# Performance work log

Hardware: AMD Instinct MI355X
Metric: run time of the kernel (lower is better)

## Reference

```python
import jax, jax.numpy as jnp
import numpy as np

N_NODES = 100000
N_EDGES = 1600000
NUM_GRAPHS = 1024
D_IN = 128
D_HID = 128
D_OUT = 2
LN_EPS = 1e-5


def setup_inputs() -> dict:
    key = jax.random.key(0)
    ks = jax.random.split(key, 10)
    x = jax.random.normal(ks[0], (N_NODES, D_IN), dtype=jnp.float32)
    edge_index = jax.random.randint(ks[1], (2, N_EDGES), 0, N_NODES, dtype=jnp.int64)
    batch = jnp.sort(jax.random.randint(ks[2], (N_NODES,), 0, NUM_GRAPHS, dtype=jnp.int64))
    s = 0.05  # weight scale to keep activations sane
    return {
        "x": x,
        "edge_index": edge_index,
        "batch": batch,
        "W1l": jax.random.normal(ks[3], (D_HID, D_IN), dtype=jnp.float32) * s,
        "b1l": jnp.zeros((D_HID,), dtype=jnp.float32),
        "W1r": jax.random.normal(ks[4], (D_HID, D_IN), dtype=jnp.float32) * s,
        "W2l": jax.random.normal(ks[5], (D_HID, D_HID), dtype=jnp.float32) * s,
        "b2l": jnp.zeros((D_HID,), dtype=jnp.float32),
        "W2r": jax.random.normal(ks[6], (D_HID, D_HID), dtype=jnp.float32) * s,
        "ln_g": jnp.ones((D_HID,), dtype=jnp.float32),
        "ln_b": jnp.zeros((D_HID,), dtype=jnp.float32),
        "Wlin": jax.random.normal(ks[7], (D_OUT, D_HID), dtype=jnp.float32) * s,
        "blin": jnp.zeros((D_OUT,), dtype=jnp.float32),
    }


def _sage_conv(x, src, dst, Wl, bl, Wr):
    # PyG SAGEConv with mean aggregation: lin_l(mean_{j in N(i)} x_j) + lin_r(x_i)
    msg_sum = jax.ops.segment_sum(x[src], dst, num_segments=N_NODES)
    deg = jax.ops.segment_sum(jnp.ones((src.shape[0], 1), x.dtype), dst, num_segments=N_NODES)
    agg = msg_sum / jnp.maximum(deg, 1.0)  # isolated nodes -> 0
    return agg @ Wl.T + bl + x @ Wr.T  # lin_r has no bias (PyG default)


def reference(x, edge_index, batch, W1l, b1l, W1r, W2l, b2l, W2r, ln_g, ln_b, Wlin, blin):
    src, dst = edge_index[0], edge_index[1]
    h = jax.nn.relu(_sage_conv(x, src, dst, W1l, b1l, W1r))
    h = jax.nn.relu(_sage_conv(h, src, dst, W2l, b2l, W2r))
    # global_add_pool over graphs
    g = jax.ops.segment_sum(h, batch, num_segments=NUM_GRAPHS)  # [G, D_HID]
    # LayerNorm over last dim
    mu = jnp.mean(g, axis=-1, keepdims=True)
    var = jnp.var(g, axis=-1, keepdims=True)
    gn = (g - mu) * jax.lax.rsqrt(var + LN_EPS) * ln_g + ln_b
    return gn @ Wlin.T + blin  # [G, D_OUT]
```

## Files before the change

### kernel.cpp

```cpp
#include <hip/hip_runtime.h>
#include <hip/hip_bf16.h>
#include <hip/hip_fp8.h>

#define N_NODES   100000
#define N_EDGES   1600000
#define NUM_GRAPHS 1024
#define D         128
#define LN_EPS    1e-5f
#define NBUCKETS  391
#define CAP       4864
#define CHUNK     4096

typedef __attribute__((ext_vector_type(8))) short short8;
typedef __attribute__((ext_vector_type(4))) float floatx4;
typedef __attribute__((ext_vector_type(2))) float f32x2;

static __device__ __forceinline__ float bf2f(unsigned int u) {
    return __uint_as_float(u << 16);
}
static __device__ __forceinline__ unsigned short f2bf(float f) {
    __hip_bfloat16 h = __float2bfloat16(f);
    return *reinterpret_cast<unsigned short*>(&h);
}
static __device__ __forceinline__ void acc4(f32x2* acc, uint4 v) {
    acc[0] += (f32x2){__uint_as_float(v.x << 16), __uint_as_float(v.x & 0xffff0000u)};
    acc[1] += (f32x2){__uint_as_float(v.y << 16), __uint_as_float(v.y & 0xffff0000u)};
    acc[2] += (f32x2){__uint_as_float(v.z << 16), __uint_as_float(v.z & 0xffff0000u)};
    acc[3] += (f32x2){__uint_as_float(v.w << 16), __uint_as_float(v.w & 0xffff0000u)};
}

#if __has_builtin(__builtin_amdgcn_cvt_pk_f32_fp8)
#define UNPK_FP8(x, w) __builtin_amdgcn_cvt_pk_f32_fp8((x), (w))
#else
static __device__ __forceinline__ f32x2 unpk_fp8_sw(unsigned x, bool w) {
    unsigned s = w ? (x >> 16) : (x & 0xffffu);
    __hip_fp8_e4m3 a, b;
    *reinterpret_cast<unsigned char*>(&a) = (unsigned char)(s & 0xff);
    *reinterpret_cast<unsigned char*>(&b) = (unsigned char)((s >> 8) & 0xff);
    return (f32x2){(float)a, (float)b};
}
#define UNPK_FP8(x, w) unpk_fp8_sw((x), (w))
#endif

#if __has_builtin(__builtin_amdgcn_cvt_pk_fp8_f32)
#define PK_FP8(a, b, old, w) ((unsigned)__builtin_amdgcn_cvt_pk_fp8_f32((a), (b), (int)(old), (w)))
#else
static __device__ __forceinline__ unsigned pk_fp8_sw(float a, float b) {
    __hip_fp8_e4m3 fa = (__hip_fp8_e4m3)a;
    __hip_fp8_e4m3 fb = (__hip_fp8_e4m3)b;
    return (unsigned)*reinterpret_cast<unsigned char*>(&fa) |
           ((unsigned)*reinterpret_cast<unsigned char*>(&fb) << 8);
}
#define PK_FP8(a, b, old, w) ((w) ? ((((unsigned)(old)) & 0xffffu) | (pk_fp8_sw((a),(b)) << 16)) \
                                  : ((((unsigned)(old)) & 0xffff0000u) | pk_fp8_sw((a),(b))))
#endif

#define GLOAD16(g, l) __builtin_amdgcn_global_load_lds( \
    (const __attribute__((address_space(1))) void*)(g), \
    (__attribute__((address_space(3))) void*)(l), 16, 0, 0)

__global__ __launch_bounds__(256)
void prep_kernel(const float* __restrict__ x, unsigned short* __restrict__ xbf,
                 unsigned* __restrict__ xf8,
                 const float* __restrict__ W1l, const float* __restrict__ W1r,
                 const float* __restrict__ W2l, const float* __restrict__ W2r,
                 unsigned short* __restrict__ Wc1, unsigned short* __restrict__ Wc2,
                 int* __restrict__ cursor) {
    int i = blockIdx.x * 256 + threadIdx.x;
    float4 v = reinterpret_cast<const float4*>(x)[i];
    ushort4 o;
    o.x = f2bf(v.x); o.y = f2bf(v.y); o.z = f2bf(v.z); o.w = f2bf(v.w);
    reinterpret_cast<ushort4*>(xbf)[i] = o;
    unsigned p = PK_FP8(v.x, v.y, 0u, false);
    p = PK_FP8(v.z, v.w, p, true);
    xf8[i] = p;
    if (blockIdx.x < 256) {
        int layer = i >> 15;
        int rem = i & 32767;
        int c = rem >> 8;
        int k = rem & 255;
        const float* Wl = layer ? W2l : W1l;
        const float* Wr = layer ? W2r : W1r;
        unsigned short* dst = layer ? Wc2 : Wc1;
        float wv = (k < 128) ? Wl[c * 128 + k] : Wr[c * 128 + (k - 128)];
        dst[c * 256 + k] = f2bf(wv);
    }
    if (blockIdx.x == 256) {
        for (int b = threadIdx.x; b < NBUCKETS; b += 256)
            cursor[b] = b * CAP;
        if (threadIdx.x < 32)
            xf8[(size_t)N_NODES * 32 + threadIdx.x] = 0u;
    }
}

__global__ __launch_bounds__(256)
void cvt_h1_kernel(const unsigned short* __restrict__ h1, uint2* __restrict__ h1f8) {
    int i = blockIdx.x * 256 + threadIdx.x;
    uint4 v = reinterpret_cast<const uint4*>(h1)[i];
    float c0 = __uint_as_float(v.x << 16), c1 = __uint_as_float(v.x & 0xffff0000u);
    float c2 = __uint_as_float(v.y << 16), c3 = __uint_as_float(v.y & 0xffff0000u);
    float c4 = __uint_as_float(v.z << 16), c5 = __uint_as_float(v.z & 0xffff0000u);
    float c6 = __uint_as_float(v.w << 16), c7 = __uint_as_float(v.w & 0xffff0000u);
    unsigned lo = PK_FP8(c0, c1, 0u, false);
    lo = PK_FP8(c2, c3, lo, true);
    unsigned hi = PK_FP8(c4, c5, 0u, false);
    hi = PK_FP8(c6, c7, hi, true);
    h1f8[i] = make_uint2(lo, hi);
}

__global__ __launch_bounds__(256)
void bin_scatter_kernel(const int* __restrict__ src, const int* __restrict__ dst,
                        int* __restrict__ cursor, unsigned* __restrict__ binned) {
    __shared__ int cnt[NBUCKETS];
    __shared__ int base[NBUCKETS];
    int chunkBase = blockIdx.x * CHUNK;
    for (int i = threadIdx.x; i < NBUCKETS; i += 256) cnt[i] = 0;
    __syncthreads();
    int es[16], ed[16], lofs[16];
    #pragma unroll
    for (int j = 0; j < 16; ++j) {
        int e = chunkBase + j * 256 + threadIdx.x;
        if (e < N_EDGES) {
            es[j] = src[e];
            ed[j] = dst[e];
            lofs[j] = atomicAdd(&cnt[ed[j] >> 8], 1);
        }
    }
    __syncthreads();
    for (int i = threadIdx.x; i < NBUCKETS; i += 256) {
        int c = cnt[i];
        base[i] = c ? atomicAdd(&cursor[i], c) : 0;
    }
    __syncthreads();
    #pragma unroll
    for (int j = 0; j < 16; ++j) {
        int e = chunkBase + j * 256 + threadIdx.x;
        if (e < N_EDGES) {
            int b = ed[j] >> 8;
            int pos = base[b] + lofs[j];
            if (pos < (b + 1) * CAP)
                binned[pos] = ((unsigned)(ed[j] & 255) << 17) | (unsigned)es[j];
        }
    }
}

__global__ __launch_bounds__(256)
void bucket_build_kernel(const unsigned* __restrict__ binned, const int* __restrict__ cursor,
                         int2* __restrict__ row_info, int* __restrict__ src_sorted) {
    __shared__ int scnt[256];
    __shared__ int sscan[256];
    int b = blockIdx.x;
    int t = threadIdx.x;
    int lo = b * CAP;
    int hi = cursor[b];
    int cap_end = lo + CAP;
    if (hi > cap_end) hi = cap_end;
    scnt[t] = 0;
    __syncthreads();
    unsigned rec[19];
    short rnk[19];
    #pragma unroll
    for (int i = 0; i < 19; ++i) {
        int e = lo + t + i * 256;
        if (e < hi) {
            unsigned r = binned[e];
            rec[i] = r;
            rnk[i] = (short)atomicAdd(&scnt[r >> 17], 1);
        }
    }
    __syncthreads();
    int v = scnt[t];
    sscan[t] = v;
    __syncthreads();
    for (int off = 1; off < 256; off <<= 1) {
        int a = (t >= off) ? sscan[t - off] : 0;
        __syncthreads();
        sscan[t] += a;
        __syncthreads();
    }
    int ex = sscan[t] - v;
    int node = b * 256 + t;
    if (node < N_NODES) row_info[node] = make_int2(lo + ex, v);
    scnt[t] = ex;
    __syncthreads();
    #pragma unroll
    for (int i = 0; i < 19; ++i) {
        int e = lo + t + i * 256;
        if (e < hi) {
            unsigned r = rec[i];
            src_sorted[lo + scnt[r >> 17] + rnk[i]] = (int)(r & 0x1FFFFu);
        }
    }
}

__global__ __launch_bounds__(256)
void aggregate_kernel(const unsigned char* __restrict__ feat8,
                      const int* __restrict__ src_sorted,
                      const int2* __restrict__ row_info,
                      unsigned short* __restrict__ aggout) {
    int bid = blockIdx.x;
    int xcd = bid & 7;
    int idx = bid >> 3;
    int lb  = (xcd < 2) ? xcd * 782 + idx : 1564 + (xcd - 2) * 781 + idx;
    int tid  = threadIdx.x;
    int wave = tid >> 6;
    int lane = tid & 63;
    int l16  = lane & 15;
    int grpbase = lane & 48;
    int node = lb * 16 + wave * 4 + (lane >> 4);
    int2 ri = row_info[node];
    int s = ri.x, deg = ri.y;
    int dmax = deg;
    dmax = max(dmax, __shfl_xor(dmax, 16, 64));
    dmax = max(dmax, __shfl_xor(dmax, 32, 64));
    unsigned chb = (unsigned)l16 * 8;
    f32x2 a0[4], a1[4];
    #pragma unroll
    for (int i = 0; i < 4; ++i) { a0[i] = (f32x2){0.f, 0.f}; a1[i] = (f32x2){0.f, 0.f}; }

    for (int c0 = 0; c0 < dmax; c0 += 16) {
        int si = src_sorted[s + c0 + l16];
        int rel = deg - c0;
        int rend = dmax - c0; if (rend > 16) rend = 16;
        int r = 0;
        for (; r + 2 <= rend; r += 2) {
            int u0 = __shfl(si, grpbase + r, 64);
            int u1 = __shfl(si, grpbase + r + 1, 64);
            u0 = (r < rel) ? u0 : N_NODES;
            u1 = (r + 1 < rel) ? u1 : N_NODES;
            uint2 v0 = *(const uint2*)(feat8 + (((unsigned)u0 << 7) + chb));
            uint2 v1 = *(const uint2*)(feat8 + (((unsigned)u1 << 7) + chb));
            a0[0] += UNPK_FP8(v0.x, false);
            a0[1] += UNPK_FP8(v0.x, true);
            a0[2] += UNPK_FP8(v0.y, false);
            a0[3] += UNPK_FP8(v0.y, true);
            a1[0] += UNPK_FP8(v1.x, false);
            a1[1] += UNPK_FP8(v1.x, true);
            a1[2] += UNPK_FP8(v1.y, false);
            a1[3] += UNPK_FP8(v1.y, true);
        }
        if (r < rend) {
            int u0 = __shfl(si, grpbase + r, 64);
            u0 = (r < rel) ? u0 : N_NODES;
            uint2 v0 = *(const uint2*)(feat8 + (((unsigned)u0 << 7) + chb));
            a0[0] += UNPK_FP8(v0.x, false);
            a0[1] += UNPK_FP8(v0.x, true);
            a0[2] += UNPK_FP8(v0.y, false);
            a0[3] += UNPK_FP8(v0.y, true);
        }
    }
    float inv = 1.f / (float)(deg > 1 ? deg : 1);
    f32x2 t0 = (a0[0] + a1[0]) * inv;
    f32x2 t1 = (a0[1] + a1[1]) * inv;
    f32x2 t2 = (a0[2] + a1[2]) * inv;
    f32x2 t3 = (a0[3] + a1[3]) * inv;
    uint4 o;
    o.x = (unsigned)f2bf(t0.x) | ((unsigned)f2bf(t0.y) << 16);
    o.y = (unsigned)f2bf(t1.x) | ((unsigned)f2bf(t1.y) << 16);
    o.z = (unsigned)f2bf(t2.x) | ((unsigned)f2bf(t2.y) << 16);
    o.w = (unsigned)f2bf(t3.x) | ((unsigned)f2bf(t3.y) << 16);
    *(uint4*)(aggout + (size_t)node * 128 + l16 * 8) = o;
}

__global__ __launch_bounds__(256)
void gemm_kernel(const unsigned short* __restrict__ A1,
                 const unsigned short* __restrict__ A2,
                 const unsigned short* __restrict__ Wcat,
                 const float* __restrict__ bias,
                 unsigned short* __restrict__ out) {
    __shared__ unsigned char sm[2][12288];
    int tid  = threadIdx.x;
    int w    = tid >> 6;
    int lane = tid & 63;
    int quad = lane >> 4, m = lane & 15;
    int nodeBase = blockIdx.x * 64;
    int gm = (m & 3) ^ ((m >> 2) & 3);
    int qo = ((quad ^ gm) & 3) * 16;

    int arow = w * 16 + (lane >> 2);
    int ga   = (arow & 3) ^ ((arow >> 2) & 3);
    int ua   = (lane & 3) ^ ga;
    int ra   = nodeBase + arow; if (ra > N_NODES - 1) ra = N_NODES - 1;
    int col0 = w * 32 + (lane >> 2);
    int col1 = col0 + 16;
    int u0 = (lane & 3) ^ ((col0 & 3) ^ ((col0 >> 2) & 3));
    int u1 = (lane & 3) ^ ((col1 & 3) ^ ((col1 >> 2) & 3));
    const char* a1c = (const char*)A1;
    const char* a2c = (const char*)A2;
    const char* wcc = (const char*)Wcat;

    floatx4 acc[4][2];
    #pragma unroll
    for (int a = 0; a < 4; ++a)
        #pragma unroll
        for (int b = 0; b < 2; ++b) acc[a][b] = (floatx4){0.f, 0.f, 0.f, 0.f};

#define STAGE(kc, buf) do {                                                      \
        const char* asrc = ((kc) < 4) ? a1c : a2c;                               \
        int kb = ((kc) & 3) * 64;                                               \
        GLOAD16(asrc + (size_t)ra * 256 + kb + ua * 16, &sm[buf][w * 1024]);     \
        int kw = (kc) * 64;                                                     \
        GLOAD16(wcc + (size_t)col0 * 512 + kw + u0 * 16, &sm[buf][4096 + (w*2)*1024]);     \
        GLOAD16(wcc + (size_t)col1 * 512 + kw + u1 * 16, &sm[buf][4096 + (w*2+1)*1024]);   \
    } while (0)

    STAGE(0, 0);
    __syncthreads();
    #pragma unroll
    for (int kc = 0; kc < 8; ++kc) {
        int buf = kc & 1;
        if (kc < 7) STAGE(kc + 1, buf ^ 1);
        const char* As = (const char*)&sm[buf][0];
        const char* Ws = (const char*)&sm[buf][4096];
        short8 afr[4], bfr[2];
        #pragma unroll
        for (int nb = 0; nb < 4; ++nb)
            afr[nb] = *(const short8*)(As + (nb * 16 + m) * 64 + qo);
        #pragma unroll
        for (int cb = 0; cb < 2; ++cb)
            bfr[cb] = *(const short8*)(Ws + (w * 32 + cb * 16 + m) * 64 + qo);
        #pragma unroll
        for (int nb = 0; nb < 4; ++nb)
            #pragma unroll
            for (int cb = 0; cb < 2; ++cb)
                acc[nb][cb] = __builtin_amdgcn_mfma_f32_16x16x32_bf16(afr[nb], bfr[cb], acc[nb][cb], 0, 0, 0);
        if (kc < 7) __syncthreads();
    }
#undef STAGE

    #pragma unroll
    for (int cb = 0; cb < 2; ++cb) {
        int col = w * 32 + cb * 16 + m;
        float bv = bias[col];
        #pragma unroll
        for (int nb = 0; nb < 4; ++nb) {
            #pragma unroll
            for (int rr = 0; rr < 4; ++rr) {
                int row = nodeBase + nb * 16 + quad * 4 + rr;
                if (row < N_NODES) {
                    float v = acc[nb][cb][rr] + bv;
                    v = v > 0.f ? v : 0.f;
                    out[(size_t)row * 128 + col] = f2bf(v);
                }
            }
        }
    }
}

__global__ __launch_bounds__(256)
void pool_ln_out_kernel(const unsigned short* __restrict__ h2,
                        const int* __restrict__ batch,
                        const float* __restrict__ ln_g, const float* __restrict__ ln_b,
                        const float* __restrict__ Wlin, const float* __restrict__ blin,
                        float* __restrict__ out) {
    int g = blockIdx.x;
    int t = threadIdx.x;
    int lane = t & 63, w = t >> 6;
    __shared__ int se[2];
    if (t < 2) {
        int target = g + t;
        int lo = 0, hi = N_NODES;
        while (lo < hi) {
            int mid = (lo + hi) >> 1;
            if (batch[mid] < target) lo = mid + 1; else hi = mid;
        }
        se[t] = lo;
    }
    __syncthreads();
    int s = se[0], e = se[1];
    int ns = t >> 4;
    int chg = t & 15;
    f32x2 a[4];
    a[0] = a[1] = a[2] = a[3] = (f32x2){0.f, 0.f};
    for (int n = s + ns; n < e; n += 16) {
        uint4 v = *(const uint4*)(h2 + (size_t)n * 128 + chg * 8);
        acc4(a, v);
    }
    #pragma unroll
    for (int i = 0; i < 4; ++i) {
        a[i].x += __shfl_xor(a[i].x, 16, 64);
        a[i].y += __shfl_xor(a[i].y, 16, 64);
        a[i].x += __shfl_xor(a[i].x, 32, 64);
        a[i].y += __shfl_xor(a[i].y, 32, 64);
    }
    __shared__ float sw[4][128];
    if (lane < 16) {
        #pragma unroll
        for (int k = 0; k < 4; ++k) {
            sw[w][chg * 8 + 2 * k]     = a[k].x;
            sw[w][chg * 8 + 2 * k + 1] = a[k].y;
        }
    }
    __syncthreads();
    __shared__ float red[128];
    float sum = 0.f;
    if (t < 128) {
        sum = sw[0][t] + sw[1][t] + sw[2][t] + sw[3][t];
        red[t] = sum;
    }
    __syncthreads();
    for (int off = 64; off > 0; off >>= 1) {
        if (t < off) red[t] += red[t + off];
        __syncthreads();
    }
    float mu = red[0] * (1.f / 128.f);
    __syncthreads();
    float dv = sum - mu;
    if (t < 128) red[t] = dv * dv;
    __syncthreads();
    for (int off = 64; off > 0; off >>= 1) {
        if (t < off) red[t] += red[t + off];
        __syncthreads();
    }
    float var = red[0] * (1.f / 128.f);
    __syncthreads();
    __shared__ float r0[128], r1[128];
    if (t < 128) {
        float gn = dv * rsqrtf(var + LN_EPS) * ln_g[t] + ln_b[t];
        r0[t] = gn * Wlin[t];
        r1[t] = gn * Wlin[128 + t];
    }
    __syncthreads();
    for (int off = 64; off > 0; off >>= 1) {
        if (t < off) { r0[t] += r0[t + off]; r1[t] += r1[t + off]; }
        __syncthreads();
    }
    if (t == 0) {
        out[g * 2 + 0] = r0[0] + blin[0];
        out[g * 2 + 1] = r1[0] + blin[1];
    }
}

extern "C" void kernel_launch(void* const* d_in, const int* in_sizes, int n_in,
                              void* d_out, int out_size, void* d_ws, size_t ws_size,
                              hipStream_t stream) {
    const float* x    = (const float*)d_in[0];
    const int*   ei   = (const int*)d_in[1];
    const int*   batch= (const int*)d_in[2];
    const float* W1l  = (const float*)d_in[3];
    const float* b1l  = (const float*)d_in[4];
    const float* W1r  = (const float*)d_in[5];
    const float* W2l  = (const float*)d_in[6];
    const float* b2l  = (const float*)d_in[7];
    const float* W2r  = (const float*)d_in[8];
    const float* ln_g = (const float*)d_in[9];
    const float* ln_b = (const float*)d_in[10];
    const float* Wlin = (const float*)d_in[11];
    const float* blin = (const float*)d_in[12];
    float* out = (float*)d_out;

    char* ws = (char*)d_ws;
    size_t off = 0;
    auto alloc = [&](size_t bytes) {
        char* p = ws + off;
        off = (off + bytes + 255) & ~(size_t)255;
        return p;
    };
    unsigned short* xbf  = (unsigned short*)alloc((size_t)N_NODES * D * 2);
    unsigned short* aggb = (unsigned short*)alloc((size_t)N_NODES * D * 2);
    unsigned short* h1   = (unsigned short*)alloc((size_t)N_NODES * D * 2);
    unsigned*       xf8  = (unsigned*)alloc((size_t)N_NODES * D + 128);
    unsigned short* Wc1  = (unsigned short*)alloc(128 * 256 * 2);
    unsigned short* Wc2  = (unsigned short*)alloc(128 * 256 * 2);
    int2* row_info   = (int2*)alloc((size_t)N_NODES * 8);
    int* src_sorted  = (int*)alloc(((size_t)NBUCKETS * CAP + 8192) * 4);
    int* cursor      = (int*)alloc(NBUCKETS * 4);
    unsigned* binned = (unsigned*)aggb;
    uint2* h1f8      = (uint2*)xf8;

    const int* srcI = ei;
    const int* dstI = ei + N_EDGES;

    prep_kernel<<<12500, 256, 0, stream>>>(x, xbf, xf8, W1l, W1r, W2l, W2r, Wc1, Wc2, cursor);
    bin_scatter_kernel<<<(N_EDGES + CHUNK - 1) / CHUNK, 256, 0, stream>>>(srcI, dstI, cursor, binned);
    bucket_build_kernel<<<NBUCKETS, 256, 0, stream>>>(binned, cursor, row_info, src_sorted);

    aggregate_kernel<<<6250, 256, 0, stream>>>((const unsigned char*)xf8, src_sorted, row_info, aggb);
    gemm_kernel<<<1563, 256, 0, stream>>>(aggb, xbf, Wc1, b1l, h1);
    cvt_h1_kernel<<<6250, 256, 0, stream>>>(h1, h1f8);
    aggregate_kernel<<<6250, 256, 0, stream>>>((const unsigned char*)h1f8, src_sorted, row_info, aggb);
    gemm_kernel<<<1563, 256, 0, stream>>>(aggb, h1, Wc2, b2l, xbf);
    pool_ln_out_kernel<<<NUM_GRAPHS, 256, 0, stream>>>(xbf, batch, ln_g, ln_b, Wlin, blin, out);
}
```

Before: 291.2 us.

## Fuse neighbor aggregation into the SAGE GEMM kernel and drop the h1 FP8 conversion

Each of the two layers now runs as one kernel: a block gathers and averages neighbor features for its 64 nodes into shared memory, then runs the MFMA GEMM against the concatenated weights. This removes the round trip of the aggregated bf16 matrix through global memory and one kernel launch per layer. The separate h1-to-FP8 conversion is also dropped, so layer 2 gathers bf16 h1 directly. That doubles the gather bytes for layer 2, and with 32KB of LDS plus the weight buffers per block, fewer blocks may be resident on each CU to hide gather latency.

Result: slower. 359.2 us (+23.3%).

```diff
diff --git a/kernel.cpp b/kernel.cpp
--- a/kernel.cpp
+++ b/kernel.cpp
@@ -15,9 +15,6 @@
 typedef __attribute__((ext_vector_type(4))) float floatx4;
 typedef __attribute__((ext_vector_type(2))) float f32x2;
 
-static __device__ __forceinline__ float bf2f(unsigned int u) {
-    return __uint_as_float(u << 16);
-}
 static __device__ __forceinline__ unsigned short f2bf(float f) {
     __hip_bfloat16 h = __float2bfloat16(f);
     return *reinterpret_cast<unsigned short*>(&h);
@@ -65,7 +62,7 @@
                  const float* __restrict__ W1l, const float* __restrict__ W1r,
                  const float* __restrict__ W2l, const float* __restrict__ W2r,
                  unsigned short* __restrict__ Wc1, unsigned short* __restrict__ Wc2,
-                 int* __restrict__ cursor) {
+                 int* __restrict__ cursor, unsigned short* __restrict__ h1) {
     int i = blockIdx.x * 256 + threadIdx.x;
     float4 v = reinterpret_cast<const float4*>(x)[i];
     ushort4 o;
@@ -90,22 +87,9 @@
             cursor[b] = b * CAP;
         if (threadIdx.x < 32)
             xf8[(size_t)N_NODES * 32 + threadIdx.x] = 0u;
-    }
-}
-
-__global__ __launch_bounds__(256)
-void cvt_h1_kernel(const unsigned short* __restrict__ h1, uint2* __restrict__ h1f8) {
-    int i = blockIdx.x * 256 + threadIdx.x;
-    uint4 v = reinterpret_cast<const uint4*>(h1)[i];
-    float c0 = __uint_as_float(v.x << 16), c1 = __uint_as_float(v.x & 0xffff0000u);
-    float c2 = __uint_as_float(v.y << 16), c3 = __uint_as_float(v.y & 0xffff0000u);
-    float c4 = __uint_as_float(v.z << 16), c5 = __uint_as_float(v.z & 0xffff0000u);
-    float c6 = __uint_as_float(v.w << 16), c7 = __uint_as_float(v.w & 0xffff0000u);
-    unsigned lo = PK_FP8(c0, c1, 0u, false);
-    lo = PK_FP8(c2, c3, lo, true);
-    unsigned hi = PK_FP8(c4, c5, 0u, false);
-    hi = PK_FP8(c6, c7, hi, true);
-    h1f8[i] = make_uint2(lo, hi);
+        if (threadIdx.x < 64)
+            reinterpret_cast<unsigned*>(h1)[(size_t)N_NODES * 64 + threadIdx.x] = 0u;
+    }
 }
 
 __global__ __launch_bounds__(256)
@@ -193,101 +177,126 @@
     }
 }
 
+template <bool FP8>
 __global__ __launch_bounds__(256)
-void aggregate_kernel(const unsigned char* __restrict__ feat8,
-                      const int* __restrict__ src_sorted,
-                      const int2* __restrict__ row_info,
-                      unsigned short* __restrict__ aggout) {
-    int bid = blockIdx.x;
-    int xcd = bid & 7;
-    int idx = bid >> 3;
-    int lb  = (xcd < 2) ? xcd * 782 + idx : 1564 + (xcd - 2) * 781 + idx;
-    int tid  = threadIdx.x;
-    int wave = tid >> 6;
-    int lane = tid & 63;
-    int l16  = lane & 15;
-    int grpbase = lane & 48;
-    int node = lb * 16 + wave * 4 + (lane >> 4);
-    int2 ri = row_info[node];
-    int s = ri.x, deg = ri.y;
-    int dmax = deg;
-    dmax = max(dmax, __shfl_xor(dmax, 16, 64));
-    dmax = max(dmax, __shfl_xor(dmax, 32, 64));
-    unsigned chb = (unsigned)l16 * 8;
-    f32x2 a0[4], a1[4];
-    #pragma unroll
-    for (int i = 0; i < 4; ++i) { a0[i] = (f32x2){0.f, 0.f}; a1[i] = (f32x2){0.f, 0.f}; }
-
-    for (int c0 = 0; c0 < dmax; c0 += 16) {
-        int si = src_sorted[s + c0 + l16];
-        int rel = deg - c0;
-        int rend = dmax - c0; if (rend > 16) rend = 16;
-        int r = 0;
-        for (; r + 2 <= rend; r += 2) {
-            int u0 = __shfl(si, grpbase + r, 64);
-            int u1 = __shfl(si, grpbase + r + 1, 64);
-            u0 = (r < rel) ? u0 : N_NODES;
-            u1 = (r + 1 < rel) ? u1 : N_NODES;
-            uint2 v0 = *(const uint2*)(feat8 + (((unsigned)u0 << 7) + chb));
-            uint2 v1 = *(const uint2*)(feat8 + (((unsigned)u1 << 7) + chb));
-            a0[0] += UNPK_FP8(v0.x, false);
-            a0[1] += UNPK_FP8(v0.x, true);
-            a0[2] += UNPK_FP8(v0.y, false);
-            a0[3] += UNPK_FP8(v0.y, true);
-            a1[0] += UNPK_FP8(v1.x, false);
-            a1[1] += UNPK_FP8(v1.x, true);
-            a1[2] += UNPK_FP8(v1.y, false);
-            a1[3] += UNPK_FP8(v1.y, true);
-        }
-        if (r < rend) {
-            int u0 = __shfl(si, grpbase + r, 64);
-            u0 = (r < rel) ? u0 : N_NODES;
-            uint2 v0 = *(const uint2*)(feat8 + (((unsigned)u0 << 7) + chb));
-            a0[0] += UNPK_FP8(v0.x, false);
-            a0[1] += UNPK_FP8(v0.x, true);
-            a0[2] += UNPK_FP8(v0.y, false);
-            a0[3] += UNPK_FP8(v0.y, true);
-        }
-    }
-    float inv = 1.f / (float)(deg > 1 ? deg : 1);
-    f32x2 t0 = (a0[0] + a1[0]) * inv;
-    f32x2 t1 = (a0[1] + a1[1]) * inv;
-    f32x2 t2 = (a0[2] + a1[2]) * inv;
-    f32x2 t3 = (a0[3] + a1[3]) * inv;
-    uint4 o;
-    o.x = (unsigned)f2bf(t0.x) | ((unsigned)f2bf(t0.y) << 16);
-    o.y = (unsigned)f2bf(t1.x) | ((unsigned)f2bf(t1.y) << 16);
-    o.z = (unsigned)f2bf(t2.x) | ((unsigned)f2bf(t2.y) << 16);
-    o.w = (unsigned)f2bf(t3.x) | ((unsigned)f2bf(t3.y) << 16);
-    *(uint4*)(aggout + (size_t)node * 128 + l16 * 8) = o;
-}
-
-__global__ __launch_bounds__(256)
-void gemm_kernel(const unsigned short* __restrict__ A1,
-                 const unsigned short* __restrict__ A2,
-                 const unsigned short* __restrict__ Wcat,
-                 const float* __restrict__ bias,
-                 unsigned short* __restrict__ out) {
-    __shared__ unsigned char sm[2][12288];
+void fused_layer_kernel(const unsigned char* __restrict__ gat,
+                        const unsigned short* __restrict__ selfA,
+                        const unsigned short* __restrict__ Wcat,
+                        const float* __restrict__ bias,
+                        const int* __restrict__ src_sorted,
+                        const int2* __restrict__ row_info,
+                        unsigned short* __restrict__ out) {
+    __shared__ unsigned char A1s[16384];
+    __shared__ unsigned char A2s[16384];
+    __shared__ unsigned char Wsm[2][8192];
     int tid  = threadIdx.x;
     int w    = tid >> 6;
     int lane = tid & 63;
     int quad = lane >> 4, m = lane & 15;
-    int nodeBase = blockIdx.x * 64;
+    int sub  = quad;
+    int l16  = m;
+    int grpbase = lane & 48;
+    int bid = blockIdx.x;
+    int xcd = bid & 7, idx = bid >> 3;
+    int lb = (xcd < 3) ? xcd * 196 + idx : 588 + (xcd - 3) * 195 + idx;
+    int nodeBase = lb * 64;
+
+    const char* wcc = (const char*)Wcat;
     int gm = (m & 3) ^ ((m >> 2) & 3);
     int qo = ((quad ^ gm) & 3) * 16;
-
-    int arow = w * 16 + (lane >> 2);
-    int ga   = (arow & 3) ^ ((arow >> 2) & 3);
-    int ua   = (lane & 3) ^ ga;
-    int ra   = nodeBase + arow; if (ra > N_NODES - 1) ra = N_NODES - 1;
     int col0 = w * 32 + (lane >> 2);
     int col1 = col0 + 16;
     int u0 = (lane & 3) ^ ((col0 & 3) ^ ((col0 >> 2) & 3));
     int u1 = (lane & 3) ^ ((col1 & 3) ^ ((col1 >> 2) & 3));
-    const char* a1c = (const char*)A1;
-    const char* a2c = (const char*)A2;
-    const char* wcc = (const char*)Wcat;
+
+#define STAGE_W(kc, buf) do {                                                    \
+        int kw = (kc) * 64;                                                      \
+        GLOAD16(wcc + (size_t)col0 * 512 + kw + u0 * 16, &Wsm[buf][(w*2)*1024]);     \
+        GLOAD16(wcc + (size_t)col1 * 512 + kw + u1 * 16, &Wsm[buf][(w*2+1)*1024]);   \
+    } while (0)
+
+    {
+        const char* sc = (const char*)selfA;
+        #pragma unroll
+        for (int j = 0; j < 4; ++j) {
+            int row = w * 16 + j * 4 + (lane >> 4);
+            int node = nodeBase + row; if (node > N_NODES - 1) node = N_NODES - 1;
+            int u = (lane & 15) ^ (row & 15);
+            GLOAD16(sc + (size_t)node * 256 + u * 16, &A2s[w * 4096 + j * 1024]);
+        }
+        STAGE_W(0, 0);
+    }
+
+    for (int round = 0; round < 4; ++round) {
+        int arow = w * 16 + round * 4 + sub;
+        int node = nodeBase + arow;
+        int nn = node < N_NODES ? node : N_NODES - 1;
+        int2 ri = row_info[nn];
+        int s = ri.x;
+        int deg = node < N_NODES ? ri.y : 0;
+        int dmax = deg;
+        dmax = max(dmax, __shfl_xor(dmax, 16, 64));
+        dmax = max(dmax, __shfl_xor(dmax, 32, 64));
+        f32x2 a0[4], a1[4];
+        #pragma unroll
+        for (int i = 0; i < 4; ++i) { a0[i] = (f32x2){0.f, 0.f}; a1[i] = (f32x2){0.f, 0.f}; }
+
+        for (int c0 = 0; c0 < dmax; c0 += 16) {
+            int si = src_sorted[s + c0 + l16];
+            int rel = deg - c0;
+            int rend = dmax - c0; if (rend > 16) rend = 16;
+            int r = 0;
+            for (; r + 2 <= rend; r += 2) {
+                int e0 = __shfl(si, grpbase + r, 64);
+                int e1 = __shfl(si, grpbase + r + 1, 64);
+                e0 = (r < rel) ? e0 : N_NODES;
+                e1 = (r + 1 < rel) ? e1 : N_NODES;
+                if constexpr (FP8) {
+                    uint2 v0 = *(const uint2*)(gat + (((size_t)e0 << 7) + l16 * 8));
+                    uint2 v1 = *(const uint2*)(gat + (((size_t)e1 << 7) + l16 * 8));
+                    a0[0] += UNPK_FP8(v0.x, false);
+                    a0[1] += UNPK_FP8(v0.x, true);
+                    a0[2] += UNPK_FP8(v0.y, false);
+                    a0[3] += UNPK_FP8(v0.y, true);
+                    a1[0] += UNPK_FP8(v1.x, false);
+                    a1[1] += UNPK_FP8(v1.x, true);
+                    a1[2] += UNPK_FP8(v1.y, false);
+                    a1[3] += UNPK_FP8(v1.y, true);
+                } else {
+                    uint4 v0 = *(const uint4*)(gat + (((size_t)e0 << 8) + l16 * 16));
+                    uint4 v1 = *(const uint4*)(gat + (((size_t)e1 << 8) + l16 * 16));
+                    acc4(a0, v0);
+                    acc4(a1, v1);
+                }
+            }
+            if (r < rend) {
+                int e0 = __shfl(si, grpbase + r, 64);
+                e0 = (r < rel) ? e0 : N_NODES;
+                if constexpr (FP8) {
+                    uint2 v0 = *(const uint2*)(gat + (((size_t)e0 << 7) + l16 * 8));
+                    a0[0] += UNPK_FP8(v0.x, false);
+                    a0[1] += UNPK_FP8(v0.x, true);
+                    a0[2] += UNPK_FP8(v0.y, false);
+                    a0[3] += UNPK_FP8(v0.y, true);
+                } else {
+                    uint4 v0 = *(const uint4*)(gat + (((size_t)e0 << 8) + l16 * 16));
+                    acc4(a0, v0);
+                }
+            }
+        }
+        float inv = 1.f / (float)(deg > 1 ? deg : 1);
+        f32x2 t0 = (a0[0] + a1[0]) * inv;
+        f32x2 t1 = (a0[1] + a1[1]) * inv;
+        f32x2 t2 = (a0[2] + a1[2]) * inv;
+        f32x2 t3 = (a0[3] + a1[3]) * inv;
+        uint4 o;
+        o.x = (unsigned)f2bf(t0.x) | ((unsigned)f2bf(t0.y) << 16);
+        o.y = (unsigned)f2bf(t1.x) | ((unsigned)f2bf(t1.y) << 16);
+        o.z = (unsigned)f2bf(t2.x) | ((unsigned)f2bf(t2.y) << 16);
+        o.w = (unsigned)f2bf(t3.x) | ((unsigned)f2bf(t3.y) << 16);
+        *(uint4*)(&A1s[arow * 256 + ((l16 ^ (arow & 15)) << 4)]) = o;
+    }
+    __syncthreads();
 
     floatx4 acc[4][2];
     #pragma unroll
@@ -295,30 +304,19 @@
         #pragma unroll
         for (int b = 0; b < 2; ++b) acc[a][b] = (floatx4){0.f, 0.f, 0.f, 0.f};
 
-#define STAGE(kc, buf) do {                                                      \
-        const char* asrc = ((kc) < 4) ? a1c : a2c;                               \
-        int kb = ((kc) & 3) * 64;                                               \
-        GLOAD16(asrc + (size_t)ra * 256 + kb + ua * 16, &sm[buf][w * 1024]);     \
-        int kw = (kc) * 64;                                                     \
-        GLOAD16(wcc + (size_t)col0 * 512 + kw + u0 * 16, &sm[buf][4096 + (w*2)*1024]);     \
-        GLOAD16(wcc + (size_t)col1 * 512 + kw + u1 * 16, &sm[buf][4096 + (w*2+1)*1024]);   \
-    } while (0)
-
-    STAGE(0, 0);
-    __syncthreads();
     #pragma unroll
     for (int kc = 0; kc < 8; ++kc) {
         int buf = kc & 1;
-        if (kc < 7) STAGE(kc + 1, buf ^ 1);
-        const char* As = (const char*)&sm[buf][0];
-        const char* Ws = (const char*)&sm[buf][4096];
+        if (kc < 7) STAGE_W(kc + 1, buf ^ 1);
+        const unsigned char* As = (kc < 4) ? A1s : A2s;
+        int ub = (kc & 3) * 4 + quad;
         short8 afr[4], bfr[2];
         #pragma unroll
         for (int nb = 0; nb < 4; ++nb)
-            afr[nb] = *(const short8*)(As + (nb * 16 + m) * 64 + qo);
+            afr[nb] = *(const short8*)(As + (nb * 16 + m) * 256 + ((ub ^ m) << 4));
         #pragma unroll
         for (int cb = 0; cb < 2; ++cb)
-            bfr[cb] = *(const short8*)(Ws + (w * 32 + cb * 16 + m) * 64 + qo);
+            bfr[cb] = *(const short8*)(&Wsm[buf][(w * 32 + cb * 16 + m) * 64 + qo]);
         #pragma unroll
         for (int nb = 0; nb < 4; ++nb)
             #pragma unroll
@@ -326,7 +324,7 @@
                 acc[nb][cb] = __builtin_amdgcn_mfma_f32_16x16x32_bf16(afr[nb], bfr[cb], acc[nb][cb], 0, 0, 0);
         if (kc < 7) __syncthreads();
     }
-#undef STAGE
+#undef STAGE_W
 
     #pragma unroll
     for (int cb = 0; cb < 2; ++cb) {
@@ -457,28 +455,25 @@
         return p;
     };
     unsigned short* xbf  = (unsigned short*)alloc((size_t)N_NODES * D * 2);
-    unsigned short* aggb = (unsigned short*)alloc((size_t)N_NODES * D * 2);
-    unsigned short* h1   = (unsigned short*)alloc((size_t)N_NODES * D * 2);
+    unsigned short* h1   = (unsigned short*)alloc(((size_t)N_NODES + 1) * D * 2);
     unsigned*       xf8  = (unsigned*)alloc((size_t)N_NODES * D + 128);
     unsigned short* Wc1  = (unsigned short*)alloc(128 * 256 * 2);
     unsigned short* Wc2  = (unsigned short*)alloc(128 * 256 * 2);
     int2* row_info   = (int2*)alloc((size_t)N_NODES * 8);
     int* src_sorted  = (int*)alloc(((size_t)NBUCKETS * CAP + 8192) * 4);
     int* cursor      = (int*)alloc(NBUCKETS * 4);
-    unsigned* binned = (unsigned*)aggb;
-    uint2* h1f8      = (uint2*)xf8;
+    unsigned* binned = (unsigned*)h1;
 
     const int* srcI = ei;
     const int* dstI = ei + N_EDGES;
 
-    prep_kernel<<<12500, 256, 0, stream>>>(x, xbf, xf8, W1l, W1r, W2l, W2r, Wc1, Wc2, cursor);
+    prep_kernel<<<12500, 256, 0, stream>>>(x, xbf, xf8, W1l, W1r, W2l, W2r, Wc1, Wc2, cursor, h1);
     bin_scatter_kernel<<<(N_EDGES + CHUNK - 1) / CHUNK, 256, 0, stream>>>(srcI, dstI, cursor, binned);
     bucket_build_kernel<<<NBUCKETS, 256, 0, stream>>>(binned, cursor, row_info, src_sorted);
 
-    aggregate_kernel<<<6250, 256, 0, stream>>>((const unsigned char*)xf8, src_sorted, row_info, aggb);
-    gemm_kernel<<<1563, 256, 0, stream>>>(aggb, xbf, Wc1, b1l, h1);
-    cvt_h1_kernel<<<6250, 256, 0, stream>>>(h1, h1f8);
-    aggregate_kernel<<<6250, 256, 0, stream>>>((const unsigned char*)h1f8, src_sorted, row_info, aggb);
-    gemm_kernel<<<1563, 256, 0, stream>>>(aggb, h1, Wc2, b2l, xbf);
+    fused_layer_kernel<true><<<1563, 256, 0, stream>>>(
+        (const unsigned char*)xf8, xbf, Wc1, b1l, src_sorted, row_info, h1);
+    fused_layer_kernel<false><<<1563, 256, 0, stream>>>(
+        (const unsigned char*)h1, h1, Wc2, b2l, src_sorted, row_info, xbf);
     pool_ln_out_kernel<<<NUM_GRAPHS, 256, 0, stream>>>(xbf, batch, ln_g, ln_b, Wlin, blin, out);
 }
```

## Sort nodes by degree for aggregation and fuse fp8 conversion into GEMM epilogue

Applied to the files above, without the earlier changes.

Builds a degree histogram during bucket construction and a new perm kernel that orders nodes by in-degree, so each aggregation wave handles nodes of similar degree and divergence from uneven neighbor counts drops. The first GEMM now also writes an fp8 copy of h1 directly, which removes the separate cvt_h1 pass and one full read of h1. In exchange there is an extra small kernel plus global atomics, the XCD-aware block remapping is dropped, and the fp8 stores in the epilogue are byte-wide and uncoalesced.

New measurement: 807.5 us. 177% more time.

```diff
diff --git a/kernel.cpp b/kernel.cpp
--- a/kernel.cpp
+++ b/kernel.cpp
@@ -15,12 +15,13 @@
 typedef __attribute__((ext_vector_type(4))) float floatx4;
 typedef __attribute__((ext_vector_type(2))) float f32x2;
 
-static __device__ __forceinline__ float bf2f(unsigned int u) {
-    return __uint_as_float(u << 16);
-}
 static __device__ __forceinline__ unsigned short f2bf(float f) {
     __hip_bfloat16 h = __float2bfloat16(f);
     return *reinterpret_cast<unsigned short*>(&h);
+}
+static __device__ __forceinline__ unsigned char fp8b(float v) {
+    __hip_fp8_e4m3 t = (__hip_fp8_e4m3)v;
+    return *reinterpret_cast<unsigned char*>(&t);
 }
 static __device__ __forceinline__ void acc4(f32x2* acc, uint4 v) {
     acc[0] += (f32x2){__uint_as_float(v.x << 16), __uint_as_float(v.x & 0xffff0000u)};
@@ -65,7 +66,7 @@
                  const float* __restrict__ W1l, const float* __restrict__ W1r,
                  const float* __restrict__ W2l, const float* __restrict__ W2r,
                  unsigned short* __restrict__ Wc1, unsigned short* __restrict__ Wc2,
-                 int* __restrict__ cursor) {
+                 int* __restrict__ cursor, int* __restrict__ dhist) {
     int i = blockIdx.x * 256 + threadIdx.x;
     float4 v = reinterpret_cast<const float4*>(x)[i];
     ushort4 o;
@@ -90,22 +91,9 @@
             cursor[b] = b * CAP;
         if (threadIdx.x < 32)
             xf8[(size_t)N_NODES * 32 + threadIdx.x] = 0u;
-    }
-}
-
-__global__ __launch_bounds__(256)
-void cvt_h1_kernel(const unsigned short* __restrict__ h1, uint2* __restrict__ h1f8) {
-    int i = blockIdx.x * 256 + threadIdx.x;
-    uint4 v = reinterpret_cast<const uint4*>(h1)[i];
-    float c0 = __uint_as_float(v.x << 16), c1 = __uint_as_float(v.x & 0xffff0000u);
-    float c2 = __uint_as_float(v.y << 16), c3 = __uint_as_float(v.y & 0xffff0000u);
-    float c4 = __uint_as_float(v.z << 16), c5 = __uint_as_float(v.z & 0xffff0000u);
-    float c6 = __uint_as_float(v.w << 16), c7 = __uint_as_float(v.w & 0xffff0000u);
-    unsigned lo = PK_FP8(c0, c1, 0u, false);
-    lo = PK_FP8(c2, c3, lo, true);
-    unsigned hi = PK_FP8(c4, c5, 0u, false);
-    hi = PK_FP8(c6, c7, hi, true);
-    h1f8[i] = make_uint2(lo, hi);
+        if (threadIdx.x < 128)
+            dhist[threadIdx.x] = 0;
+    }
 }
 
 __global__ __launch_bounds__(256)
@@ -146,7 +134,8 @@
 
 __global__ __launch_bounds__(256)
 void bucket_build_kernel(const unsigned* __restrict__ binned, const int* __restrict__ cursor,
-                         int2* __restrict__ row_info, int* __restrict__ src_sorted) {
+                         int2* __restrict__ row_info, int* __restrict__ src_sorted,
+                         int* __restrict__ dhist) {
     __shared__ int scnt[256];
     __shared__ int sscan[256];
     int b = blockIdx.x;
@@ -180,7 +169,10 @@
     }
     int ex = sscan[t] - v;
     int node = b * 256 + t;
-    if (node < N_NODES) row_info[node] = make_int2(lo + ex, v);
+    if (node < N_NODES) {
+        row_info[node] = make_int2(lo + ex, v);
+        atomicAdd(&dhist[v < 63 ? v : 63], 1);
+    }
     scnt[t] = ex;
     __syncthreads();
     #pragma unroll
@@ -194,20 +186,40 @@
 }
 
 __global__ __launch_bounds__(256)
+void perm_kernel(const int2* __restrict__ row_info, const int* __restrict__ dhist,
+                 int* __restrict__ dcur, int* __restrict__ perm) {
+    __shared__ int sc[64];
+    int t = threadIdx.x;
+    if (t < 64) sc[t] = dhist[t];
+    __syncthreads();
+    for (int off = 1; off < 64; off <<= 1) {
+        int a = (t < 64 && t >= off) ? sc[t - off] : 0;
+        __syncthreads();
+        if (t < 64) sc[t] += a;
+        __syncthreads();
+    }
+    int node = blockIdx.x * 256 + t;
+    if (node < N_NODES) {
+        int dg = row_info[node].y;
+        int bin = dg < 63 ? dg : 63;
+        int base = bin ? sc[bin - 1] : 0;
+        int pos = base + atomicAdd(&dcur[bin], 1);
+        perm[pos] = node;
+    }
+}
+
+__global__ __launch_bounds__(256)
 void aggregate_kernel(const unsigned char* __restrict__ feat8,
                       const int* __restrict__ src_sorted,
                       const int2* __restrict__ row_info,
+                      const int* __restrict__ perm,
                       unsigned short* __restrict__ aggout) {
-    int bid = blockIdx.x;
-    int xcd = bid & 7;
-    int idx = bid >> 3;
-    int lb  = (xcd < 2) ? xcd * 782 + idx : 1564 + (xcd - 2) * 781 + idx;
     int tid  = threadIdx.x;
     int wave = tid >> 6;
     int lane = tid & 63;
     int l16  = lane & 15;
     int grpbase = lane & 48;
-    int node = lb * 16 + wave * 4 + (lane >> 4);
+    int node = perm[blockIdx.x * 16 + wave * 4 + (lane >> 4)];
     int2 ri = row_info[node];
     int s = ri.x, deg = ri.y;
     int dmax = deg;
@@ -267,7 +279,8 @@
                  const unsigned short* __restrict__ A2,
                  const unsigned short* __restrict__ Wcat,
                  const float* __restrict__ bias,
-                 unsigned short* __restrict__ out) {
+                 unsigned short* __restrict__ out,
+                 unsigned char* __restrict__ f8out) {
     __shared__ unsigned char sm[2][12288];
     int tid  = threadIdx.x;
     int w    = tid >> 6;
@@ -341,6 +354,7 @@
                     float v = acc[nb][cb][rr] + bv;
                     v = v > 0.f ? v : 0.f;
                     out[(size_t)row * 128 + col] = f2bf(v);
+                    if (f8out) f8out[(size_t)row * 128 + col] = fp8b(v);
                 }
             }
         }
@@ -465,20 +479,23 @@
     int2* row_info   = (int2*)alloc((size_t)N_NODES * 8);
     int* src_sorted  = (int*)alloc(((size_t)NBUCKETS * CAP + 8192) * 4);
     int* cursor      = (int*)alloc(NBUCKETS * 4);
+    int* dhist       = (int*)alloc(128 * 4);
+    int* dcur        = dhist + 64;
+    int* perm        = (int*)alloc((size_t)N_NODES * 4);
     unsigned* binned = (unsigned*)aggb;
-    uint2* h1f8      = (uint2*)xf8;
+    unsigned char* h1f8 = (unsigned char*)xf8;
 
     const int* srcI = ei;
     const int* dstI = ei + N_EDGES;
 
-    prep_kernel<<<12500, 256, 0, stream>>>(x, xbf, xf8, W1l, W1r, W2l, W2r, Wc1, Wc2, cursor);
+    prep_kernel<<<12500, 256, 0, stream>>>(x, xbf, xf8, W1l, W1r, W2l, W2r, Wc1, Wc2, cursor, dhist);
     bin_scatter_kernel<<<(N_EDGES + CHUNK - 1) / CHUNK, 256, 0, stream>>>(srcI, dstI, cursor, binned);
-    bucket_build_kernel<<<NBUCKETS, 256, 0, stream>>>(binned, cursor, row_info, src_sorted);
-
-    aggregate_kernel<<<6250, 256, 0, stream>>>((const unsigned char*)xf8, src_sorted, row_info, aggb);
-    gemm_kernel<<<1563, 256, 0, stream>>>(aggb, xbf, Wc1, b1l, h1);
-    cvt_h1_kernel<<<6250, 256, 0, stream>>>(h1, h1f8);
-    aggregate_kernel<<<6250, 256, 0, stream>>>((const unsigned char*)h1f8, src_sorted, row_info, aggb);
-    gemm_kernel<<<1563, 256, 0, stream>>>(aggb, h1, Wc2, b2l, xbf);
+    bucket_build_kernel<<<NBUCKETS, 256, 0, stream>>>(binned, cursor, row_info, src_sorted, dhist);
+    perm_kernel<<<NBUCKETS, 256, 0, stream>>>(row_info, dhist, dcur, perm);
+
+    aggregate_kernel<<<6250, 256, 0, stream>>>((const unsigned char*)xf8, src_sorted, row_info, perm, aggb);
+    gemm_kernel<<<1563, 256, 0, stream>>>(aggb, xbf, Wc1, b1l, h1, h1f8);
+    aggregate_kernel<<<6250, 256, 0, stream>>>(h1f8, src_sorted, row_info, perm, aggb);
+    gemm_kernel<<<1563, 256, 0, stream>>>(aggb, h1, Wc2, b2l, xbf, nullptr);
     pool_ln_out_kernel<<<NUM_GRAPHS, 256, 0, stream>>>(xbf, batch, ln_g, ln_b, Wlin, blin, out);
 }
```
